# Performance work log

Measured on AMD Instinct MI355X. Metric: run time of the kernel, lower is better.

## Reference

```python
import jax, jax.numpy as jnp
import numpy as np
from jax import lax

B, S, D, H, O = 128, 256, 128, 512, 25
TEMP = 0.1


def _init(key, shape, scale):
    return jax.random.uniform(key, shape, jnp.float32, -scale, scale)


def setup_inputs() -> dict:
    key = jax.random.key(0)
    ks = jax.random.split(key, 24)
    sH = 1.0 / np.sqrt(H)
    s2H = 1.0 / np.sqrt(2 * H)
    sD = 1.0 / np.sqrt(D)
    inp = {
        "x": jax.random.normal(ks[0], (B, S, D), jnp.float32),
        "noise_u": jnp.clip(jax.random.uniform(ks[1], (S, B, 1), jnp.float32), 1e-6, 1 - 1e-6),
        # layer_cin: Linear(D, H)
        "w_cin": _init(ks[2], (D, H), sD), "b_cin": _init(ks[3], (H,), sD),
        # layer_c MLP: 2H->2H (x3, ReLU) -> 1
        "w1": _init(ks[4], (2 * H, 2 * H), s2H), "b1": _init(ks[5], (2 * H,), s2H),
        "w2": _init(ks[6], (2 * H, 2 * H), s2H), "b2": _init(ks[7], (2 * H,), s2H),
        "w3": _init(ks[8], (2 * H, 2 * H), s2H), "b3": _init(ks[9], (2 * H,), s2H),
        "w4": _init(ks[10], (2 * H, 1), s2H), "b4": _init(ks[11], (1,), s2H),
        # GRUCell(H, H): gates ordered (r, z, n)
        "w_ih": _init(ks[12], (H, 3 * H), sH), "b_ih": _init(ks[13], (3 * H,), sH),
        "w_hh": _init(ks[14], (H, 3 * H), sH), "b_hh": _init(ks[15], (3 * H,), sH),
        # output Linear(H, O)
        "w_out": _init(ks[16], (H, O), sH), "b_out": _init(ks[17], (O,), sH),
    }
    return inp


def _gru_cell(x, h, w_ih, b_ih, w_hh, b_hh):
    gx = x @ w_ih + b_ih  # [B, 3H]
    gh = h @ w_hh + b_hh
    xr, xz, xn = jnp.split(gx, 3, axis=-1)
    hr, hz, hn = jnp.split(gh, 3, axis=-1)
    r = jax.nn.sigmoid(xr + hr)
    z = jax.nn.sigmoid(xz + hz)
    n = jnp.tanh(xn + r * hn)
    return (1.0 - z) * n + z * h


def reference(x, noise_u, w_cin, b_cin, w1, b1, w2, b2, w3, b3, w4, b4,
              w_ih, b_ih, w_hh, b_hh, w_out, b_out):
    xs = jnp.transpose(x, (1, 0, 2))  # [S, B, D]

    def step(carry, inp):
        c, h, n = carry
        x_t, u = inp
        c_in = jnp.tanh(x_t @ w_cin + b_cin)  # [B, H]
        com = jnp.concatenate([c, c_in], axis=1)  # [B, 2H]
        z = jax.nn.relu(com @ w1 + b1)
        z = jax.nn.relu(z @ w2 + b2)
        z = jax.nn.relu(z @ w3 + b3)
        alpha_logit = z @ w4 + b4  # [B, 1]
        # RelaxedBernoulli(temp=0.1).sample(): sigmoid((logits + logistic noise)/T), detached
        logistic = jnp.log(u) - jnp.log1p(-u)
        alpha = lax.stop_gradient(jax.nn.sigmoid((alpha_logit + logistic) / TEMP))
        h_gru = _gru_cell(c, h, w_ih, b_ih, w_hh, b_hh)
        h_new = h * (1.0 - alpha) + alpha * h_gru
        new_n = n * (1.0 - alpha) + 1.0
        c_new = (c * n * (1.0 - alpha) + c_in) / new_n
        return (c_new, h_new, new_n), None

    c0 = jnp.zeros((B, H), x.dtype)
    h0 = jnp.zeros((B, H), x.dtype)
    n0 = jnp.zeros((B, 1), x.dtype)
    (c, h, n), _ = lax.scan(step, (c0, h0, n0), (xs, noise_u))
    h = _gru_cell(c, h, w_ih, b_ih, w_hh, b_hh)  # final post-loop GRU step
    return h @ w_out + b_out
```

## Files before the change

kernel.cpp:

```cpp
#include <hip/hip_runtime.h>
#include <math.h>

#define SLEN 256
#define BSZ  128
#define DIN  128
#define HSZ  512
#define HH2  1024
#define GG3  1536
#define OSZ  25

typedef _Float16 h8 __attribute__((ext_vector_type(8)));
typedef float    f4 __attribute__((ext_vector_type(4)));

struct P_t {
  const float *x, *noise, *b_cin, *b1, *b2, *b3, *w4, *b4, *b_ih, *b_hh, *w_out, *b_out;
  _Float16 *WT1, *WT2, *WT3, *WTih, *WThh, *WTcin;
  _Float16 *FW1, *FW2, *FW3, *FWih, *FWhh;
  _Float16 *CIN, *COMlo, *Z1, *Z2, *HF16;
  float *LOGI, *GX, *GH, *PART, *HF32, *CF32, *NF32;
  float *out;
};

__device__ __forceinline__ f4 mfma16(h8 a, h8 b, f4 c) {
  return __builtin_amdgcn_mfma_f32_16x16x32_f16(a, b, c, 0, 0, 0);
}

__global__ __launch_bounds__(256) void transpose_cvt(const float* __restrict__ src,
    _Float16* __restrict__ dst, int K, int N) {
  __shared__ float tl[32][33];
  int nt = N >> 5;
  int bx = blockIdx.x % nt, by = blockIdx.x / nt;
  int n0 = bx << 5, k0 = by << 5;
  int tx = threadIdx.x & 31, ty = threadIdx.x >> 5;
#pragma unroll
  for (int i = 0; i < 4; ++i) {
    int r = ty + (i << 3);
    tl[r][tx] = src[(size_t)(k0 + r) * N + n0 + tx];
  }
  __syncthreads();
#pragma unroll
  for (int i = 0; i < 4; ++i) {
    int r = ty + (i << 3);
    dst[(size_t)(n0 + r) * K + k0 + tx] = (_Float16)tl[tx][r];
  }
}

__global__ __launch_bounds__(512) void fragpack(const _Float16* __restrict__ src,
    _Float16* __restrict__ dst, int K) {
  int ct = blockIdx.x;
  int chunks = (K / 32) * 64;
  for (int idx = threadIdx.x; idx < chunks; idx += 512) {
    int i = idx >> 6, lane = idx & 63;
    int mlw = lane & 15, qw = lane >> 4;
    *(h8*)(dst + ((size_t)ct * (K / 32) + i) * 512 + (size_t)lane * 8) =
        *(const h8*)(src + ((size_t)ct * 16 + mlw) * K + i * 32 + qw * 8);
  }
}

__global__ __launch_bounds__(256) void cin_kernel(P_t P) {
  int tid = blockIdx.x * blockDim.x + threadIdx.x;
  if (tid < SLEN * BSZ) {
    float u = P.noise[tid];
    P.LOGI[tid] = logf(u) - log1pf(-u);
  }
  int gw = tid >> 6, lane = tid & 63;
  int nw = (gridDim.x * blockDim.x) >> 6;
  int ml = lane & 15, q = lane >> 4;
  const int MT = (SLEN * BSZ) / 16;
  for (int tt = gw; tt < MT * 8; tt += nw) {
    int mt = tt & (MT - 1), nt = tt / MT;
    int m0 = mt * 16, n0 = nt * 64;
    int m = m0 + ml, b = m & 127, s = m >> 7;
    const float* ap = P.x + ((size_t)b * SLEN + s) * DIN + q * 8;
    const _Float16* bp = P.WTcin + (size_t)(n0 + ml) * DIN + q * 8;
    f4 a0 = {0,0,0,0}, a1 = a0, a2 = a0, a3 = a0;
#pragma unroll
    for (int k = 0; k < DIN; k += 32) {
      f4 lo = *(const f4*)(ap + k);
      f4 hi = *(const f4*)(ap + k + 4);
      h8 av;
      av[0] = (_Float16)lo[0]; av[1] = (_Float16)lo[1];
      av[2] = (_Float16)lo[2]; av[3] = (_Float16)lo[3];
      av[4] = (_Float16)hi[0]; av[5] = (_Float16)hi[1];
      av[6] = (_Float16)hi[2]; av[7] = (_Float16)hi[3];
      a0 = mfma16(av, *(const h8*)(bp + k),            a0);
      a1 = mfma16(av, *(const h8*)(bp + 16*DIN + k),   a1);
      a2 = mfma16(av, *(const h8*)(bp + 32*DIN + k),   a2);
      a3 = mfma16(av, *(const h8*)(bp + 48*DIN + k),   a3);
    }
#pragma unroll
    for (int r = 0; r < 4; ++r) {
      int row = m0 + q * 4 + r;
      int c0 = n0 + ml;
      P.CIN[(size_t)row * HSZ + c0     ] = (_Float16)tanhf(a0[r] + P.b_cin[c0]);
      P.CIN[(size_t)row * HSZ + c0 + 16] = (_Float16)tanhf(a1[r] + P.b_cin[c0 + 16]);
      P.CIN[(size_t)row * HSZ + c0 + 32] = (_Float16)tanhf(a2[r] + P.b_cin[c0 + 32]);
      P.CIN[(size_t)row * HSZ + c0 + 48] = (_Float16)tanhf(a3[r] + P.b_cin[c0 + 48]);
    }
  }
}

__global__ __launch_bounds__(256) void init_kernel(P_t P) {
  int idx = blockIdx.x * 256 + threadIdx.x;
  if (idx < BSZ * HSZ) {
    P.HF32[idx] = 0.f; P.CF32[idx] = 0.f;
    P.HF16[idx] = (_Float16)0.f; P.COMlo[idx] = (_Float16)0.f;
  }
  if (idx < BSZ) P.NF32[idx] = 0.f;
}

__global__ __launch_bounds__(256) void step_a(P_t P, int t, int base) {
  const int tid = threadIdx.x;
  const int lane = tid & 63, wv = tid >> 6;
  const int ml = lane & 15, q = lane >> 4;
  const int g = base + blockIdx.x * 4 + wv;
  f4 acc = {0.f, 0.f, 0.f, 0.f};
  if (g < 512) {
    int rt = g & 7, ct = g >> 3;
    int m0 = rt * 16, col = ct * 16 + ml;
    const _Float16* a0 = P.COMlo + (size_t)(m0 + ml) * HSZ + q * 8;
    const _Float16* a1 = P.CIN + ((size_t)t * BSZ + m0 + ml) * HSZ + q * 8;
    const _Float16* bp = P.FW1 + (size_t)ct * 32 * 512 + (size_t)lane * 8;
#pragma unroll
    for (int i = 0; i < 16; ++i)
      acc = mfma16(*(const h8*)(a0 + i * 32), *(const h8*)(bp + (size_t)i * 512), acc);
#pragma unroll
    for (int i = 0; i < 16; ++i)
      acc = mfma16(*(const h8*)(a1 + i * 32), *(const h8*)(bp + (size_t)(16 + i) * 512), acc);
    float bia = P.b1[col];
#pragma unroll
    for (int j = 0; j < 4; ++j)
      P.Z1[(size_t)(m0 + q * 4 + j) * HH2 + col] = (_Float16)fmaxf(acc[j] + bia, 0.f);
  } else if (g < 1280) {
    int u = g - 512, rt = u & 7, ct = u >> 3;
    int m0 = rt * 16, col = ct * 16 + ml;
    const _Float16* a0 = P.COMlo + (size_t)(m0 + ml) * HSZ + q * 8;
    const _Float16* bp = P.FWih + (size_t)ct * 16 * 512 + (size_t)lane * 8;
#pragma unroll
    for (int i = 0; i < 16; ++i)
      acc = mfma16(*(const h8*)(a0 + i * 32), *(const h8*)(bp + (size_t)i * 512), acc);
    float bia = P.b_ih[col];
#pragma unroll
    for (int j = 0; j < 4; ++j)
      P.GX[(size_t)(m0 + q * 4 + j) * GG3 + col] = acc[j] + bia;
  } else {
    int u = g - 1280, rt = u & 7, ct = u >> 3;
    int m0 = rt * 16, col = ct * 16 + ml;
    const _Float16* a0 = P.HF16 + (size_t)(m0 + ml) * HSZ + q * 8;
    const _Float16* bp = P.FWhh + (size_t)ct * 16 * 512 + (size_t)lane * 8;
#pragma unroll
    for (int i = 0; i < 16; ++i)
      acc = mfma16(*(const h8*)(a0 + i * 32), *(const h8*)(bp + (size_t)i * 512), acc);
    float bia = P.b_hh[col];
#pragma unroll
    for (int j = 0; j < 4; ++j)
      P.GH[(size_t)(m0 + q * 4 + j) * GG3 + col] = acc[j] + bia;
  }
}

__global__ __launch_bounds__(256) void step_b(P_t P) {
  const int tid = threadIdx.x;
  const int lane = tid & 63, wv = tid >> 6;
  const int ml = lane & 15, q = lane >> 4;
  const int g = blockIdx.x * 4 + wv;
  int rt = g & 7, ct = g >> 3;
  int m0 = rt * 16, col = ct * 16 + ml;
  const _Float16* a0 = P.Z1 + (size_t)(m0 + ml) * HH2 + q * 8;
  const _Float16* bp = P.FW2 + (size_t)ct * 32 * 512 + (size_t)lane * 8;
  f4 acc = {0.f, 0.f, 0.f, 0.f};
#pragma unroll
  for (int i = 0; i < 32; ++i)
    acc = mfma16(*(const h8*)(a0 + i * 32), *(const h8*)(bp + (size_t)i * 512), acc);
  float bia = P.b2[col];
#pragma unroll
  for (int j = 0; j < 4; ++j)
    P.Z2[(size_t)(m0 + q * 4 + j) * HH2 + col] = (_Float16)fmaxf(acc[j] + bia, 0.f);
}

__global__ __launch_bounds__(256) void step_c(P_t P) {
  const int tid = threadIdx.x;
  const int lane = tid & 63, wv = tid >> 6;
  const int ml = lane & 15, q = lane >> 4;
  const int g = blockIdx.x * 4 + wv;
  int rt = g & 7, ct = g >> 3;
  int m0 = rt * 16, col = ct * 16 + ml;
  const _Float16* a0 = P.Z2 + (size_t)(m0 + ml) * HH2 + q * 8;
  const _Float16* bp = P.FW3 + (size_t)ct * 32 * 512 + (size_t)lane * 8;
  f4 acc = {0.f, 0.f, 0.f, 0.f};
#pragma unroll
  for (int i = 0; i < 32; ++i)
    acc = mfma16(*(const h8*)(a0 + i * 32), *(const h8*)(bp + (size_t)i * 512), acc);
  float bia = P.b3[col], w4v = P.w4[col];
#pragma unroll
  for (int j = 0; j < 4; ++j) {
    float v = fmaxf(acc[j] + bia, 0.f) * w4v;
    v += __shfl_xor(v, 1); v += __shfl_xor(v, 2);
    v += __shfl_xor(v, 4); v += __shfl_xor(v, 8);
    if (ml == 0) P.PART[(size_t)ct * BSZ + m0 + q * 4 + j] = v;
  }
}

__global__ __launch_bounds__(512) void step_d(P_t P, int t) {
  __shared__ float sa[4];
  const int r = blockIdx.x, tid = threadIdx.x;
  if (tid < 64) {
    float v = P.PART[(size_t)tid * BSZ + r];
#pragma unroll
    for (int off = 32; off > 0; off >>= 1) v += __shfl_xor(v, off);
    if (tid == 0) {
      float lg = (v + P.b4[0] + P.LOGI[(size_t)t * BSZ + r]) * 10.0f;
      float alpha = 1.f / (1.f + expf(-lg));
      float om = 1.f - alpha;
      float n_old = P.NF32[r];
      float nnew = n_old * om + 1.f;
      P.NF32[r] = nnew;
      sa[0] = alpha; sa[1] = om; sa[2] = n_old * om; sa[3] = nnew;
    }
  }
  __syncthreads();
  float alpha = sa[0], om = sa[1], nom = sa[2], nnew = sa[3];
  int col = tid;
  size_t go = (size_t)r * GG3 + col;
  float xr = P.GX[go], xz = P.GX[go + 512], xn = P.GX[go + 1024];
  float hr = P.GH[go], hz = P.GH[go + 512], hn = P.GH[go + 1024];
  float rg = 1.f / (1.f + expf(-(xr + hr)));
  float zg = 1.f / (1.f + expf(-(xz + hz)));
  float ng = tanhf(xn + rg * hn);
  size_t ho = (size_t)r * HSZ + col;
  float h_old = P.HF32[ho];
  float hg = (1.f - zg) * ng + zg * h_old;
  float hnew = h_old * om + alpha * hg;
  P.HF32[ho] = hnew; P.HF16[ho] = (_Float16)hnew;
  float c_old = P.CF32[ho];
  float cin_t = (float)P.CIN[((size_t)t * BSZ + r) * HSZ + col];
  float cnew = (c_old * nom + cin_t) / nnew;
  P.CF32[ho] = cnew; P.COMlo[ho] = (_Float16)cnew;
}

__global__ __launch_bounds__(512) void final_kernel(P_t P) {
  __shared__ float hf[512];
  const int r = blockIdx.x, tid = threadIdx.x;
  const int lane = tid & 63, wv = tid >> 6;
  {
    int col = tid;
    size_t go = (size_t)r * GG3 + col;
    float xr = P.GX[go], xz = P.GX[go + 512], xn = P.GX[go + 1024];
    float hr = P.GH[go], hz = P.GH[go + 512], hn = P.GH[go + 1024];
    float rg = 1.f / (1.f + expf(-(xr + hr)));
    float zg = 1.f / (1.f + expf(-(xz + hz)));
    float ng = tanhf(xn + rg * hn);
    float h_old = P.HF32[(size_t)r * HSZ + col];
    hf[col] = (1.f - zg) * ng + zg * h_old;
  }
  __syncthreads();
  for (int c = wv; c < OSZ; c += 8) {
    float v = 0.f;
#pragma unroll
    for (int j = 0; j < 8; ++j)
      v += hf[lane + 64 * j] * P.w_out[(size_t)(lane + 64 * j) * OSZ + c];
#pragma unroll
    for (int off = 32; off > 0; off >>= 1) v += __shfl_xor(v, off);
    if (lane == 0) P.out[r * OSZ + c] = v + P.b_out[c];
  }
}

extern "C" void kernel_launch(void* const* d_in, const int* in_sizes, int n_in,
                              void* d_out, int out_size, void* d_ws, size_t ws_size,
                              hipStream_t stream) {
  const float* x     = (const float*)d_in[0];
  const float* noise = (const float*)d_in[1];
  const float* w_cin = (const float*)d_in[2];
  const float* b_cin = (const float*)d_in[3];
  const float* w1    = (const float*)d_in[4];
  const float* b1    = (const float*)d_in[5];
  const float* w2    = (const float*)d_in[6];
  const float* b2    = (const float*)d_in[7];
  const float* w3    = (const float*)d_in[8];
  const float* b3    = (const float*)d_in[9];
  const float* w4    = (const float*)d_in[10];
  const float* b4    = (const float*)d_in[11];
  const float* w_ih  = (const float*)d_in[12];
  const float* b_ih  = (const float*)d_in[13];
  const float* w_hh  = (const float*)d_in[14];
  const float* b_hh  = (const float*)d_in[15];
  const float* w_out = (const float*)d_in[16];
  const float* b_out = (const float*)d_in[17];

  char* ws = (char*)d_ws;
  size_t off = 0;
  auto alloc = [&](size_t bytes) -> void* {
    void* p = ws + off;
    off = (off + bytes + 255) & ~(size_t)255;
    return p;
  };

  P_t P;
  P.x = x; P.noise = noise; P.b_cin = b_cin; P.b1 = b1; P.b2 = b2; P.b3 = b3;
  P.w4 = w4; P.b4 = b4; P.b_ih = b_ih; P.b_hh = b_hh; P.w_out = w_out; P.b_out = b_out;
  P.WT1   = (_Float16*)alloc((size_t)HH2 * HH2 * 2);
  P.WT2   = (_Float16*)alloc((size_t)HH2 * HH2 * 2);
  P.WT3   = (_Float16*)alloc((size_t)HH2 * HH2 * 2);
  P.WTih  = (_Float16*)alloc((size_t)GG3 * HSZ * 2);
  P.WThh  = (_Float16*)alloc((size_t)GG3 * HSZ * 2);
  P.WTcin = (_Float16*)alloc((size_t)HSZ * DIN * 2);
  P.FW1   = (_Float16*)alloc((size_t)HH2 * HH2 * 2);
  P.FW2   = (_Float16*)alloc((size_t)HH2 * HH2 * 2);
  P.FW3   = (_Float16*)alloc((size_t)HH2 * HH2 * 2);
  P.FWih  = (_Float16*)alloc((size_t)GG3 * HSZ * 2);
  P.FWhh  = (_Float16*)alloc((size_t)GG3 * HSZ * 2);
  P.CIN   = (_Float16*)alloc((size_t)SLEN * BSZ * HSZ * 2);
  P.COMlo = (_Float16*)alloc((size_t)BSZ * HSZ * 2);
  P.Z1    = (_Float16*)alloc((size_t)BSZ * HH2 * 2);
  P.Z2    = (_Float16*)alloc((size_t)BSZ * HH2 * 2);
  P.HF16  = (_Float16*)alloc((size_t)BSZ * HSZ * 2);
  P.LOGI  = (float*)alloc((size_t)SLEN * BSZ * 4);
  P.GX    = (float*)alloc((size_t)BSZ * GG3 * 4);
  P.GH    = (float*)alloc((size_t)BSZ * GG3 * 4);
  P.PART  = (float*)alloc((size_t)64 * BSZ * 4);
  P.HF32  = (float*)alloc((size_t)BSZ * HSZ * 4);
  P.CF32  = (float*)alloc((size_t)BSZ * HSZ * 4);
  P.NF32  = (float*)alloc((size_t)BSZ * 4);
  P.out   = (float*)d_out;

  transpose_cvt<<<(HH2/32)*(HH2/32), 256, 0, stream>>>(w1, P.WT1, HH2, HH2);
  transpose_cvt<<<(HH2/32)*(HH2/32), 256, 0, stream>>>(w2, P.WT2, HH2, HH2);
  transpose_cvt<<<(HH2/32)*(HH2/32), 256, 0, stream>>>(w3, P.WT3, HH2, HH2);
  transpose_cvt<<<(GG3/32)*(HSZ/32), 256, 0, stream>>>(w_ih, P.WTih, HSZ, GG3);
  transpose_cvt<<<(GG3/32)*(HSZ/32), 256, 0, stream>>>(w_hh, P.WThh, HSZ, GG3);
  transpose_cvt<<<(HSZ/32)*(DIN/32), 256, 0, stream>>>(w_cin, P.WTcin, DIN, HSZ);
  fragpack<<<HH2/16, 512, 0, stream>>>(P.WT1, P.FW1, HH2);
  fragpack<<<HH2/16, 512, 0, stream>>>(P.WT2, P.FW2, HH2);
  fragpack<<<HH2/16, 512, 0, stream>>>(P.WT3, P.FW3, HH2);
  fragpack<<<GG3/16, 512, 0, stream>>>(P.WTih, P.FWih, HSZ);
  fragpack<<<GG3/16, 512, 0, stream>>>(P.WThh, P.FWhh, HSZ);

  cin_kernel<<<1024, 256, 0, stream>>>(P);
  init_kernel<<<256, 256, 0, stream>>>(P);

  for (int t = 0; t < SLEN; ++t) {
    step_a<<<512, 256, 0, stream>>>(P, t, 0);
    step_b<<<128, 256, 0, stream>>>(P);
    step_c<<<128, 256, 0, stream>>>(P);
    step_d<<<BSZ, 512, 0, stream>>>(P, t);
  }
  step_a<<<384, 256, 0, stream>>>(P, 0, 512);
  final_kernel<<<BSZ, 512, 0, stream>>>(P);
}
```

Measured before the change: 7.152 ms.

## Restructure recurrence with linear accumulators and fuse step kernels into two per step

Rewrites the per-step recurrence algebraically. Because c is a running weighted mean of c_in, its products with W1 and W_ih are kept as accumulators (A1, AIH) updated with the alpha decay. These accumulators, along with the GRU hidden-state products, replace the per-step c matmuls, and the next step's c_in contribution to layer 1 is precomputed. Four launches per step drop to two. The second kernel merges layer 3, the alpha reduction (through an atomic counter spin barrier across blocks), the layer-1 activation and the GRU update. This adds extra fp32 state traffic, a spin-wait with a timeout that could silently break correctness, and changes in numerical rounding.

```diff
diff --git a/kernel.cpp b/kernel.cpp
--- a/kernel.cpp
+++ b/kernel.cpp
@@ -8,16 +8,20 @@
 #define HH2  1024
 #define GG3  1536
 #define OSZ  25
+#define SPIN_LIMIT (1 << 22)
 
 typedef _Float16 h8 __attribute__((ext_vector_type(8)));
+typedef _Float16 h4v __attribute__((ext_vector_type(4)));
 typedef float    f4 __attribute__((ext_vector_type(4)));
 
 struct P_t {
   const float *x, *noise, *b_cin, *b1, *b2, *b3, *w4, *b4, *b_ih, *b_hh, *w_out, *b_out;
   _Float16 *WT1, *WT2, *WT3, *WTih, *WThh, *WTcin;
-  _Float16 *FW1, *FW2, *FW3, *FWih, *FWhh;
-  _Float16 *CIN, *COMlo, *Z1, *Z2, *HF16;
-  float *LOGI, *GX, *GH, *PART, *HF32, *CF32, *NF32;
+  _Float16 *FW1T, *FW1B, *FW2, *FW3, *FWih, *FWhh;
+  _Float16 *CIN, *Z1, *Z2, *HGRU16;
+  float *LOGI, *C1, *D1, *CIH, *G;
+  float *A1, *AIH, *AHH, *HF, *HGRUF, *NF, *PART;
+  int *CNT;
   float *out;
 };
 
@@ -45,15 +49,15 @@
   }
 }
 
-__global__ __launch_bounds__(512) void fragpack(const _Float16* __restrict__ src,
-    _Float16* __restrict__ dst, int K) {
+__global__ __launch_bounds__(512) void fragpack2(const _Float16* __restrict__ src,
+    _Float16* __restrict__ dst, int srcK, int kOff, int K) {
   int ct = blockIdx.x;
   int chunks = (K / 32) * 64;
   for (int idx = threadIdx.x; idx < chunks; idx += 512) {
     int i = idx >> 6, lane = idx & 63;
     int mlw = lane & 15, qw = lane >> 4;
     *(h8*)(dst + ((size_t)ct * (K / 32) + i) * 512 + (size_t)lane * 8) =
-        *(const h8*)(src + ((size_t)ct * 16 + mlw) * K + i * 32 + qw * 8);
+        *(const h8*)(src + ((size_t)ct * 16 + mlw) * srcK + kOff + i * 32 + qw * 8);
   }
 }
 
@@ -102,163 +106,233 @@
 
 __global__ __launch_bounds__(256) void init_kernel(P_t P) {
   int idx = blockIdx.x * 256 + threadIdx.x;
-  if (idx < BSZ * HSZ) {
-    P.HF32[idx] = 0.f; P.CF32[idx] = 0.f;
-    P.HF16[idx] = (_Float16)0.f; P.COMlo[idx] = (_Float16)0.f;
-  }
-  if (idx < BSZ) P.NF32[idx] = 0.f;
-}
-
-__global__ __launch_bounds__(256) void step_a(P_t P, int t, int base) {
-  const int tid = threadIdx.x;
-  const int lane = tid & 63, wv = tid >> 6;
+  for (int i = idx; i < BSZ * GG3; i += 65536) { P.AIH[i] = 0.f; P.AHH[i] = 0.f; }
+  for (int i = idx; i < BSZ * HH2; i += 65536) P.A1[i] = 0.f;
+  if (idx < BSZ * HSZ) P.HF[idx] = 0.f;
+  if (idx < 2 * BSZ) P.NF[idx] = 0.f;
+  if (idx < 128) P.CNT[idx] = 0;
+}
+
+__global__ __launch_bounds__(256) void boot_kernel(P_t P) {
+  const int tid = threadIdx.x, lane = tid & 63, wv = tid >> 6;
   const int ml = lane & 15, q = lane >> 4;
-  const int g = base + blockIdx.x * 4 + wv;
+  const int g = blockIdx.x * 4 + wv;
+  {
+    int rt = g & 7, ct = g >> 3, m0 = rt << 4, col = (ct << 4) + ml;
+    const _Float16* a0 = P.CIN + (size_t)(m0 + ml) * HSZ + q * 8;
+    const _Float16* bp = P.FW1B + (size_t)ct * 16 * 512 + (size_t)lane * 8;
+    f4 acc = {0.f, 0.f, 0.f, 0.f};
+#pragma unroll
+    for (int k = 0; k < 16; ++k)
+      acc = mfma16(*(const h8*)(a0 + k * 32), *(const h8*)(bp + (size_t)k * 512), acc);
+    float bia = P.b1[col];
+#pragma unroll
+    for (int j = 0; j < 4; ++j)
+      P.Z1[(size_t)(m0 + q * 4 + j) * HH2 + col] = (_Float16)fmaxf(acc[j] + bia, 0.f);
+  }
+  int e = blockIdx.x * 512 + tid;
+#pragma unroll
+  for (int rep = 0; rep < 2; ++rep, e += 256) {
+    int row = e >> 9, cc = e & 511;
+    float rg = 1.f / (1.f + expf(-(P.b_ih[cc] + P.b_hh[cc])));
+    float zg = 1.f / (1.f + expf(-(P.b_ih[cc + 512] + P.b_hh[cc + 512])));
+    float ng = tanhf(P.b_ih[cc + 1024] + rg * P.b_hh[cc + 1024]);
+    float v = (1.f - zg) * ng;
+    P.HGRUF[(size_t)row * HSZ + cc] = v;
+    P.HGRU16[(size_t)row * HSZ + cc] = (_Float16)v;
+  }
+}
+
+__global__ __launch_bounds__(256) void node_a(P_t P, int t) {
+  const int tid = threadIdx.x, lane = tid & 63, wv = tid >> 6;
+  const int ml = lane & 15, q = lane >> 4;
+  const int g = blockIdx.x * 4 + wv;
   f4 acc = {0.f, 0.f, 0.f, 0.f};
   if (g < 512) {
-    int rt = g & 7, ct = g >> 3;
-    int m0 = rt * 16, col = ct * 16 + ml;
-    const _Float16* a0 = P.COMlo + (size_t)(m0 + ml) * HSZ + q * 8;
-    const _Float16* a1 = P.CIN + ((size_t)t * BSZ + m0 + ml) * HSZ + q * 8;
-    const _Float16* bp = P.FW1 + (size_t)ct * 32 * 512 + (size_t)lane * 8;
-#pragma unroll
-    for (int i = 0; i < 16; ++i)
-      acc = mfma16(*(const h8*)(a0 + i * 32), *(const h8*)(bp + (size_t)i * 512), acc);
-#pragma unroll
-    for (int i = 0; i < 16; ++i)
-      acc = mfma16(*(const h8*)(a1 + i * 32), *(const h8*)(bp + (size_t)(16 + i) * 512), acc);
-    float bia = P.b1[col];
+    int rt = g & 7, ct = g >> 3, m0 = rt << 4, col = (ct << 4) + ml;
+    const _Float16* a0 = P.Z1 + (size_t)(m0 + ml) * HH2 + q * 8;
+    const _Float16* bp = P.FW2 + (size_t)ct * 32 * 512 + (size_t)lane * 8;
+#pragma unroll
+    for (int k = 0; k < 32; ++k)
+      acc = mfma16(*(const h8*)(a0 + k * 32), *(const h8*)(bp + (size_t)k * 512), acc);
+    float bia = P.b2[col];
 #pragma unroll
     for (int j = 0; j < 4; ++j)
-      P.Z1[(size_t)(m0 + q * 4 + j) * HH2 + col] = (_Float16)fmaxf(acc[j] + bia, 0.f);
+      P.Z2[(size_t)(m0 + q * 4 + j) * HH2 + col] = (_Float16)fmaxf(acc[j] + bia, 0.f);
   } else if (g < 1280) {
-    int u = g - 512, rt = u & 7, ct = u >> 3;
-    int m0 = rt * 16, col = ct * 16 + ml;
-    const _Float16* a0 = P.COMlo + (size_t)(m0 + ml) * HSZ + q * 8;
+    int u = g - 512, rt = u & 7, ct = u >> 3, m0 = rt << 4, col = (ct << 4) + ml;
+    const _Float16* a0 = P.HGRU16 + (size_t)(m0 + ml) * HSZ + q * 8;
+    const _Float16* bp = P.FWhh + (size_t)ct * 16 * 512 + (size_t)lane * 8;
+#pragma unroll
+    for (int k = 0; k < 16; ++k)
+      acc = mfma16(*(const h8*)(a0 + k * 32), *(const h8*)(bp + (size_t)k * 512), acc);
+#pragma unroll
+    for (int j = 0; j < 4; ++j)
+      P.G[(size_t)(m0 + q * 4 + j) * GG3 + col] = acc[j];
+  } else if (g < 1792) {
+    int u = g - 1280, rt = u & 7, ct = u >> 3, m0 = rt << 4, col = (ct << 4) + ml;
+    const _Float16* a0 = P.CIN + ((size_t)t * BSZ + m0 + ml) * HSZ + q * 8;
+    const _Float16* bp = P.FW1T + (size_t)ct * 16 * 512 + (size_t)lane * 8;
+#pragma unroll
+    for (int k = 0; k < 16; ++k)
+      acc = mfma16(*(const h8*)(a0 + k * 32), *(const h8*)(bp + (size_t)k * 512), acc);
+#pragma unroll
+    for (int j = 0; j < 4; ++j)
+      P.C1[(size_t)(m0 + q * 4 + j) * HH2 + col] = acc[j];
+  } else if (g < 2560) {
+    int u = g - 1792, rt = u & 7, ct = u >> 3, m0 = rt << 4, col = (ct << 4) + ml;
+    const _Float16* a0 = P.CIN + ((size_t)t * BSZ + m0 + ml) * HSZ + q * 8;
     const _Float16* bp = P.FWih + (size_t)ct * 16 * 512 + (size_t)lane * 8;
 #pragma unroll
-    for (int i = 0; i < 16; ++i)
-      acc = mfma16(*(const h8*)(a0 + i * 32), *(const h8*)(bp + (size_t)i * 512), acc);
-    float bia = P.b_ih[col];
+    for (int k = 0; k < 16; ++k)
+      acc = mfma16(*(const h8*)(a0 + k * 32), *(const h8*)(bp + (size_t)k * 512), acc);
 #pragma unroll
     for (int j = 0; j < 4; ++j)
-      P.GX[(size_t)(m0 + q * 4 + j) * GG3 + col] = acc[j] + bia;
+      P.CIH[(size_t)(m0 + q * 4 + j) * GG3 + col] = acc[j];
   } else {
-    int u = g - 1280, rt = u & 7, ct = u >> 3;
-    int m0 = rt * 16, col = ct * 16 + ml;
-    const _Float16* a0 = P.HF16 + (size_t)(m0 + ml) * HSZ + q * 8;
-    const _Float16* bp = P.FWhh + (size_t)ct * 16 * 512 + (size_t)lane * 8;
-#pragma unroll
-    for (int i = 0; i < 16; ++i)
-      acc = mfma16(*(const h8*)(a0 + i * 32), *(const h8*)(bp + (size_t)i * 512), acc);
-    float bia = P.b_hh[col];
-#pragma unroll
-    for (int j = 0; j < 4; ++j)
-      P.GH[(size_t)(m0 + q * 4 + j) * GG3 + col] = acc[j] + bia;
-  }
-}
-
-__global__ __launch_bounds__(256) void step_b(P_t P) {
-  const int tid = threadIdx.x;
-  const int lane = tid & 63, wv = tid >> 6;
+    if (t + 1 < SLEN) {
+      int u = g - 2560, rt = u & 7, ct = u >> 3, m0 = rt << 4, col = (ct << 4) + ml;
+      const _Float16* a0 = P.CIN + ((size_t)(t + 1) * BSZ + m0 + ml) * HSZ + q * 8;
+      const _Float16* bp = P.FW1B + (size_t)ct * 16 * 512 + (size_t)lane * 8;
+#pragma unroll
+      for (int k = 0; k < 16; ++k)
+        acc = mfma16(*(const h8*)(a0 + k * 32), *(const h8*)(bp + (size_t)k * 512), acc);
+#pragma unroll
+      for (int j = 0; j < 4; ++j)
+        P.D1[(size_t)(m0 + q * 4 + j) * HH2 + col] = acc[j];
+    }
+  }
+}
+
+__global__ __launch_bounds__(256) void node_b(P_t P, int t) {
+  const int tid = threadIdx.x, lane = tid & 63, wv = tid >> 6;
   const int ml = lane & 15, q = lane >> 4;
-  const int g = blockIdx.x * 4 + wv;
-  int rt = g & 7, ct = g >> 3;
-  int m0 = rt * 16, col = ct * 16 + ml;
-  const _Float16* a0 = P.Z1 + (size_t)(m0 + ml) * HH2 + q * 8;
-  const _Float16* bp = P.FW2 + (size_t)ct * 32 * 512 + (size_t)lane * 8;
-  f4 acc = {0.f, 0.f, 0.f, 0.f};
-#pragma unroll
-  for (int i = 0; i < 32; ++i)
-    acc = mfma16(*(const h8*)(a0 + i * 32), *(const h8*)(bp + (size_t)i * 512), acc);
-  float bia = P.b2[col];
-#pragma unroll
-  for (int j = 0; j < 4; ++j)
-    P.Z2[(size_t)(m0 + q * 4 + j) * HH2 + col] = (_Float16)fmaxf(acc[j] + bia, 0.f);
-}
-
-__global__ __launch_bounds__(256) void step_c(P_t P) {
-  const int tid = threadIdx.x;
-  const int lane = tid & 63, wv = tid >> 6;
-  const int ml = lane & 15, q = lane >> 4;
-  const int g = blockIdx.x * 4 + wv;
-  int rt = g & 7, ct = g >> 3;
-  int m0 = rt * 16, col = ct * 16 + ml;
-  const _Float16* a0 = P.Z2 + (size_t)(m0 + ml) * HH2 + q * 8;
-  const _Float16* bp = P.FW3 + (size_t)ct * 32 * 512 + (size_t)lane * 8;
-  f4 acc = {0.f, 0.f, 0.f, 0.f};
-#pragma unroll
-  for (int i = 0; i < 32; ++i)
-    acc = mfma16(*(const h8*)(a0 + i * 32), *(const h8*)(bp + (size_t)i * 512), acc);
-  float bia = P.b3[col], w4v = P.w4[col];
-#pragma unroll
-  for (int j = 0; j < 4; ++j) {
-    float v = fmaxf(acc[j] + bia, 0.f) * w4v;
+  const int b = blockIdx.x, rt = b & 7, sub = b >> 3;
+  const int m0 = rt << 4;
+  __shared__ float sAl[16], sNN[16];
+
+  {
+    int ct = sub * 4 + wv, col = (ct << 4) + ml;
+    const _Float16* a0 = P.Z2 + (size_t)(m0 + ml) * HH2 + q * 8;
+    const _Float16* bp = P.FW3 + (size_t)ct * 32 * 512 + (size_t)lane * 8;
+    f4 acc = {0.f, 0.f, 0.f, 0.f};
+#pragma unroll
+    for (int k = 0; k < 32; ++k)
+      acc = mfma16(*(const h8*)(a0 + k * 32), *(const h8*)(bp + (size_t)k * 512), acc);
+    float bia = P.b3[col], w4v = P.w4[col];
+#pragma unroll
+    for (int j = 0; j < 4; ++j) {
+      float v = fmaxf(acc[j] + bia, 0.f) * w4v;
+      v += __shfl_xor(v, 1); v += __shfl_xor(v, 2);
+      v += __shfl_xor(v, 4); v += __shfl_xor(v, 8);
+      if (ml == 0)
+        __hip_atomic_store(&P.PART[(size_t)ct * BSZ + m0 + q * 4 + j], v,
+                           __ATOMIC_RELAXED, __HIP_MEMORY_SCOPE_AGENT);
+    }
+  }
+  asm volatile("s_waitcnt vmcnt(0)" ::: "memory");
+  __syncthreads();
+  if (tid == 0) {
+    __hip_atomic_fetch_add(&P.CNT[rt * 16], 1, __ATOMIC_RELAXED, __HIP_MEMORY_SCOPE_AGENT);
+    const int target = 16 * (t + 1);
+    int tries = 0;
+    while (__hip_atomic_load(&P.CNT[rt * 16], __ATOMIC_RELAXED,
+                             __HIP_MEMORY_SCOPE_AGENT) < target) {
+      if (++tries > SPIN_LIMIT) break;
+      __builtin_amdgcn_s_sleep(1);
+    }
+  }
+  __syncthreads();
+
+  {
+    int rl = tid >> 4, sg = tid & 15, row = m0 + rl;
+    float v = 0.f;
+#pragma unroll
+    for (int k2 = 0; k2 < 4; ++k2)
+      v += __hip_atomic_load(&P.PART[(size_t)(sg * 4 + k2) * BSZ + row],
+                             __ATOMIC_RELAXED, __HIP_MEMORY_SCOPE_AGENT);
     v += __shfl_xor(v, 1); v += __shfl_xor(v, 2);
     v += __shfl_xor(v, 4); v += __shfl_xor(v, 8);
-    if (ml == 0) P.PART[(size_t)ct * BSZ + m0 + q * 4 + j] = v;
-  }
-}
-
-__global__ __launch_bounds__(512) void step_d(P_t P, int t) {
-  __shared__ float sa[4];
-  const int r = blockIdx.x, tid = threadIdx.x;
-  if (tid < 64) {
-    float v = P.PART[(size_t)tid * BSZ + r];
-#pragma unroll
-    for (int off = 32; off > 0; off >>= 1) v += __shfl_xor(v, off);
-    if (tid == 0) {
-      float lg = (v + P.b4[0] + P.LOGI[(size_t)t * BSZ + r]) * 10.0f;
-      float alpha = 1.f / (1.f + expf(-lg));
-      float om = 1.f - alpha;
-      float n_old = P.NF32[r];
-      float nnew = n_old * om + 1.f;
-      P.NF32[r] = nnew;
-      sa[0] = alpha; sa[1] = om; sa[2] = n_old * om; sa[3] = nnew;
+    if (sg == 0) {
+      float lg = (v + P.b4[0] + P.LOGI[(size_t)t * BSZ + row]) * 10.0f;
+      float al = 1.f / (1.f + expf(-lg));
+      float no = P.NF[((t + 1) & 1) * BSZ + row];
+      float nn = no * (1.f - al) + 1.f;
+      sAl[rl] = al; sNN[rl] = nn;
+      if (sub == 0) P.NF[(t & 1) * BSZ + row] = nn;
     }
   }
   __syncthreads();
-  float alpha = sa[0], om = sa[1], nom = sa[2], nnew = sa[3];
-  int col = tid;
-  size_t go = (size_t)r * GG3 + col;
-  float xr = P.GX[go], xz = P.GX[go + 512], xn = P.GX[go + 1024];
-  float hr = P.GH[go], hz = P.GH[go + 512], hn = P.GH[go + 1024];
-  float rg = 1.f / (1.f + expf(-(xr + hr)));
-  float zg = 1.f / (1.f + expf(-(xz + hz)));
-  float ng = tanhf(xn + rg * hn);
-  size_t ho = (size_t)r * HSZ + col;
-  float h_old = P.HF32[ho];
-  float hg = (1.f - zg) * ng + zg * h_old;
-  float hnew = h_old * om + alpha * hg;
-  P.HF32[ho] = hnew; P.HF16[ho] = (_Float16)hnew;
-  float c_old = P.CF32[ho];
-  float cin_t = (float)P.CIN[((size_t)t * BSZ + r) * HSZ + col];
-  float cnew = (c_old * nom + cin_t) / nnew;
-  P.CF32[ho] = cnew; P.COMlo[ho] = (_Float16)cnew;
-}
-
-__global__ __launch_bounds__(512) void final_kernel(P_t P) {
+
+  {
+    int rl = tid >> 4, row = m0 + rl;
+    int c0 = sub * 64 + (tid & 15) * 4;
+    float al = sAl[rl], om = 1.f - al, rin = 1.f / sNN[rl];
+    size_t o = (size_t)row * HH2 + c0;
+    f4 a = *(f4*)(P.A1 + o);
+    f4 c1 = *(const f4*)(P.C1 + o);
+#pragma unroll
+    for (int j = 0; j < 4; ++j) a[j] = om * a[j] + c1[j];
+    *(f4*)(P.A1 + o) = a;
+    if (t + 1 < SLEN) {
+      f4 d = *(const f4*)(P.D1 + o);
+      f4 bb = *(const f4*)(P.b1 + c0);
+      h4v zo;
+#pragma unroll
+      for (int j = 0; j < 4; ++j)
+        zo[j] = (_Float16)fmaxf(a[j] * rin + d[j] + bb[j], 0.f);
+      *(h4v*)(P.Z1 + o) = zo;
+    }
+  }
+
+  {
+    int rl = tid >> 4, row = m0 + rl;
+    float al = sAl[rl], om = 1.f - al, rin = 1.f / sNN[rl];
+    int cbase = sub * 32 + (tid & 15) * 2;
+#pragma unroll
+    for (int e = 0; e < 2; ++e) {
+      int cc = cbase + e;
+      size_t o3 = (size_t)row * GG3 + cc;
+      float air = om * P.AIH[o3]        + P.CIH[o3];
+      float aiz = om * P.AIH[o3 + 512]  + P.CIH[o3 + 512];
+      float ain = om * P.AIH[o3 + 1024] + P.CIH[o3 + 1024];
+      P.AIH[o3] = air; P.AIH[o3 + 512] = aiz; P.AIH[o3 + 1024] = ain;
+      float ahr = om * P.AHH[o3]        + al * P.G[o3];
+      float ahz = om * P.AHH[o3 + 512]  + al * P.G[o3 + 512];
+      float ahn = om * P.AHH[o3 + 1024] + al * P.G[o3 + 1024];
+      P.AHH[o3] = ahr; P.AHH[o3 + 512] = ahz; P.AHH[o3 + 1024] = ahn;
+      float gxr = air * rin + P.b_ih[cc];
+      float gxz = aiz * rin + P.b_ih[cc + 512];
+      float gxn = ain * rin + P.b_ih[cc + 1024];
+      float ghr = ahr + P.b_hh[cc];
+      float ghz = ahz + P.b_hh[cc + 512];
+      float ghn = ahn + P.b_hh[cc + 1024];
+      float rg = 1.f / (1.f + expf(-(gxr + ghr)));
+      float zg = 1.f / (1.f + expf(-(gxz + ghz)));
+      float ng = tanhf(gxn + rg * ghn);
+      size_t oh = (size_t)row * HSZ + cc;
+      float hold = P.HF[oh];
+      float hgt  = P.HGRUF[oh];
+      float hnew = om * hold + al * hgt;
+      P.HF[oh] = hnew;
+      float hg1 = (1.f - zg) * ng + zg * hnew;
+      P.HGRUF[oh] = hg1;
+      P.HGRU16[oh] = (_Float16)hg1;
+    }
+  }
+}
+
+__global__ __launch_bounds__(256) void final_out(P_t P) {
   __shared__ float hf[512];
   const int r = blockIdx.x, tid = threadIdx.x;
   const int lane = tid & 63, wv = tid >> 6;
-  {
-    int col = tid;
-    size_t go = (size_t)r * GG3 + col;
-    float xr = P.GX[go], xz = P.GX[go + 512], xn = P.GX[go + 1024];
-    float hr = P.GH[go], hz = P.GH[go + 512], hn = P.GH[go + 1024];
-    float rg = 1.f / (1.f + expf(-(xr + hr)));
-    float zg = 1.f / (1.f + expf(-(xz + hz)));
-    float ng = tanhf(xn + rg * hn);
-    float h_old = P.HF32[(size_t)r * HSZ + col];
-    hf[col] = (1.f - zg) * ng + zg * h_old;
-  }
+  for (int e = tid; e < 512; e += 256) hf[e] = P.HGRUF[(size_t)r * HSZ + e];
   __syncthreads();
-  for (int c = wv; c < OSZ; c += 8) {
+  for (int c = wv; c < OSZ; c += 4) {
     float v = 0.f;
 #pragma unroll
     for (int j = 0; j < 8; ++j)
       v += hf[lane + 64 * j] * P.w_out[(size_t)(lane + 64 * j) * OSZ + c];
-#pragma unroll
     for (int off = 32; off > 0; off >>= 1) v += __shfl_xor(v, off);
     if (lane == 0) P.out[r * OSZ + c] = v + P.b_out[c];
   }
@@ -297,30 +371,36 @@
   P_t P;
   P.x = x; P.noise = noise; P.b_cin = b_cin; P.b1 = b1; P.b2 = b2; P.b3 = b3;
   P.w4 = w4; P.b4 = b4; P.b_ih = b_ih; P.b_hh = b_hh; P.w_out = w_out; P.b_out = b_out;
-  P.WT1   = (_Float16*)alloc((size_t)HH2 * HH2 * 2);
-  P.WT2   = (_Float16*)alloc((size_t)HH2 * HH2 * 2);
-  P.WT3   = (_Float16*)alloc((size_t)HH2 * HH2 * 2);
-  P.WTih  = (_Float16*)alloc((size_t)GG3 * HSZ * 2);
-  P.WThh  = (_Float16*)alloc((size_t)GG3 * HSZ * 2);
-  P.WTcin = (_Float16*)alloc((size_t)HSZ * DIN * 2);
-  P.FW1   = (_Float16*)alloc((size_t)HH2 * HH2 * 2);
-  P.FW2   = (_Float16*)alloc((size_t)HH2 * HH2 * 2);
-  P.FW3   = (_Float16*)alloc((size_t)HH2 * HH2 * 2);
-  P.FWih  = (_Float16*)alloc((size_t)GG3 * HSZ * 2);
-  P.FWhh  = (_Float16*)alloc((size_t)GG3 * HSZ * 2);
-  P.CIN   = (_Float16*)alloc((size_t)SLEN * BSZ * HSZ * 2);
-  P.COMlo = (_Float16*)alloc((size_t)BSZ * HSZ * 2);
-  P.Z1    = (_Float16*)alloc((size_t)BSZ * HH2 * 2);
-  P.Z2    = (_Float16*)alloc((size_t)BSZ * HH2 * 2);
-  P.HF16  = (_Float16*)alloc((size_t)BSZ * HSZ * 2);
-  P.LOGI  = (float*)alloc((size_t)SLEN * BSZ * 4);
-  P.GX    = (float*)alloc((size_t)BSZ * GG3 * 4);
-  P.GH    = (float*)alloc((size_t)BSZ * GG3 * 4);
-  P.PART  = (float*)alloc((size_t)64 * BSZ * 4);
-  P.HF32  = (float*)alloc((size_t)BSZ * HSZ * 4);
-  P.CF32  = (float*)alloc((size_t)BSZ * HSZ * 4);
-  P.NF32  = (float*)alloc((size_t)BSZ * 4);
-  P.out   = (float*)d_out;
+  P.WT1    = (_Float16*)alloc((size_t)HH2 * HH2 * 2);
+  P.WT2    = (_Float16*)alloc((size_t)HH2 * HH2 * 2);
+  P.WT3    = (_Float16*)alloc((size_t)HH2 * HH2 * 2);
+  P.WTih   = (_Float16*)alloc((size_t)GG3 * HSZ * 2);
+  P.WThh   = (_Float16*)alloc((size_t)GG3 * HSZ * 2);
+  P.WTcin  = (_Float16*)alloc((size_t)HSZ * DIN * 2);
+  P.FW1T   = (_Float16*)alloc((size_t)HH2 * 512 * 2);
+  P.FW1B   = (_Float16*)alloc((size_t)HH2 * 512 * 2);
+  P.FW2    = (_Float16*)alloc((size_t)HH2 * HH2 * 2);
+  P.FW3    = (_Float16*)alloc((size_t)HH2 * HH2 * 2);
+  P.FWih   = (_Float16*)alloc((size_t)GG3 * HSZ * 2);
+  P.FWhh   = (_Float16*)alloc((size_t)GG3 * HSZ * 2);
+  P.CIN    = (_Float16*)alloc((size_t)SLEN * BSZ * HSZ * 2);
+  P.Z1     = (_Float16*)alloc((size_t)BSZ * HH2 * 2);
+  P.Z2     = (_Float16*)alloc((size_t)BSZ * HH2 * 2);
+  P.HGRU16 = (_Float16*)alloc((size_t)BSZ * HSZ * 2);
+  P.LOGI   = (float*)alloc((size_t)SLEN * BSZ * 4);
+  P.C1     = (float*)alloc((size_t)BSZ * HH2 * 4);
+  P.D1     = (float*)alloc((size_t)BSZ * HH2 * 4);
+  P.CIH    = (float*)alloc((size_t)BSZ * GG3 * 4);
+  P.G      = (float*)alloc((size_t)BSZ * GG3 * 4);
+  P.A1     = (float*)alloc((size_t)BSZ * HH2 * 4);
+  P.AIH    = (float*)alloc((size_t)BSZ * GG3 * 4);
+  P.AHH    = (float*)alloc((size_t)BSZ * GG3 * 4);
+  P.HF     = (float*)alloc((size_t)BSZ * HSZ * 4);
+  P.HGRUF  = (float*)alloc((size_t)BSZ * HSZ * 4);
+  P.NF     = (float*)alloc((size_t)2 * BSZ * 4);
+  P.PART   = (float*)alloc((size_t)64 * BSZ * 4);
+  P.CNT    = (int*)alloc(128 * 4);
+  P.out    = (float*)d_out;
 
   transpose_cvt<<<(HH2/32)*(HH2/32), 256, 0, stream>>>(w1, P.WT1, HH2, HH2);
   transpose_cvt<<<(HH2/32)*(HH2/32), 256, 0, stream>>>(w2, P.WT2, HH2, HH2);
@@ -328,21 +408,20 @@
   transpose_cvt<<<(GG3/32)*(HSZ/32), 256, 0, stream>>>(w_ih, P.WTih, HSZ, GG3);
   transpose_cvt<<<(GG3/32)*(HSZ/32), 256, 0, stream>>>(w_hh, P.WThh, HSZ, GG3);
   transpose_cvt<<<(HSZ/32)*(DIN/32), 256, 0, stream>>>(w_cin, P.WTcin, DIN, HSZ);
-  fragpack<<<HH2/16, 512, 0, stream>>>(P.WT1, P.FW1, HH2);
-  fragpack<<<HH2/16, 512, 0, stream>>>(P.WT2, P.FW2, HH2);
-  fragpack<<<HH2/16, 512, 0, stream>>>(P.WT3, P.FW3, HH2);
-  fragpack<<<GG3/16, 512, 0, stream>>>(P.WTih, P.FWih, HSZ);
-  fragpack<<<GG3/16, 512, 0, stream>>>(P.WThh, P.FWhh, HSZ);
+  fragpack2<<<HH2/16, 512, 0, stream>>>(P.WT1, P.FW1T, HH2, 0, 512);
+  fragpack2<<<HH2/16, 512, 0, stream>>>(P.WT1, P.FW1B, HH2, 512, 512);
+  fragpack2<<<HH2/16, 512, 0, stream>>>(P.WT2, P.FW2, HH2, 0, HH2);
+  fragpack2<<<HH2/16, 512, 0, stream>>>(P.WT3, P.FW3, HH2, 0, HH2);
+  fragpack2<<<GG3/16, 512, 0, stream>>>(P.WTih, P.FWih, HSZ, 0, HSZ);
+  fragpack2<<<GG3/16, 512, 0, stream>>>(P.WThh, P.FWhh, HSZ, 0, HSZ);
 
   cin_kernel<<<1024, 256, 0, stream>>>(P);
   init_kernel<<<256, 256, 0, stream>>>(P);
+  boot_kernel<<<128, 256, 0, stream>>>(P);
 
   for (int t = 0; t < SLEN; ++t) {
-    step_a<<<512, 256, 0, stream>>>(P, t, 0);
-    step_b<<<128, 256, 0, stream>>>(P);
-    step_c<<<128, 256, 0, stream>>>(P);
-    step_d<<<BSZ, 512, 0, stream>>>(P, t);
-  }
-  step_a<<<384, 256, 0, stream>>>(P, 0, 512);
-  final_kernel<<<BSZ, 512, 0, stream>>>(P);
-}
+    node_a<<<768, 256, 0, stream>>>(P, t);
+    node_b<<<128, 256, 0, stream>>>(P, t);
+  }
+  final_out<<<BSZ, 256, 0, stream>>>(P);
+}
```

After: 6.443 ms. -9.9%, faster.
